# Kernel tuning notes

Measured on AMD Instinct MI355X. Metric: run time of the kernel, lower is better.

Reference implementation:

```python
import jax, jax.numpy as jnp
import numpy as np


def setup_inputs() -> dict:
    key = jax.random.key(0)
    ks = jax.random.split(key, 8)
    B, N, E, d, R = 16, 4096, 65536, 256, 4
    Vg, Vs = 30000, 20000
    x = jax.random.uniform(ks[0], (B, N, d), dtype=jnp.float32)
    W_all = jax.random.normal(ks[1], (R + 1, d, d), dtype=jnp.float32)
    Wg = jax.random.normal(ks[2], (d, Vg), dtype=jnp.float32)
    bg = jnp.zeros((Vg,), dtype=jnp.float32)
    Ws = jax.random.normal(ks[3], (d, Vs), dtype=jnp.float32)
    bs = jnp.zeros((Vs,), dtype=jnp.float32)
    edge_index = jax.random.randint(ks[4], (B, 2, E), 0, N, dtype=jnp.int64)
    edge_type = jax.random.randint(ks[5], (B, E), 0, R, dtype=jnp.int64)
    return {"x": x, "W_all": W_all, "Wg": Wg, "bg": bg, "Ws": Ws, "bs": bs,
            "edge_index": edge_index, "edge_type": edge_type}


def _rgcn_graph(xg, W_all, Wg, bg, Ws, bs, ei, et):
    # xg: [N,d], ei: [2,E], et: [E]
    N, d = xg.shape
    R = W_all.shape[0] - 1
    src, dst = ei[0], ei[1]
    # per-relation support H @ W_r (relations 1..R); W_all[0] is self-connection
    support = jnp.einsum('nd,rde->rne', xg, W_all[1:])  # [R, N, d]
    # c_ir = max(#edges of relation r with source i, 1)  (row-degree of A_r)
    deg = jnp.zeros((N, R), xg.dtype).at[src, et].add(1.0)
    c = jnp.maximum(deg, 1.0)
    # edge-wise gather-scale-scatter: out[i] += support[r, j] / c[i, r]
    w = 1.0 / c[src, et]                      # [E]
    msgs = support[et, dst] * w[:, None]      # [E, d]
    agg = jax.ops.segment_sum(msgs, src, num_segments=N)  # [N, d]
    h = jax.nn.relu(agg + xg @ W_all[0])
    x0 = h[0]                                  # current node features [d]
    logits_g = x0 @ Wg + bg
    logits_s = x0 @ Ws + bs
    return jax.nn.log_softmax(logits_g), jax.nn.log_softmax(logits_s)


def reference(x, W_all, Wg, bg, Ws, bs, edge_index, edge_type):
    f = jax.vmap(_rgcn_graph, in_axes=(0, None, None, None, None, None, 0, 0))
    return f(x, W_all, Wg, bg, Ws, bs, edge_index, edge_type)
```

## Files before the change

### kernel.cpp

```cpp
#include <hip/hip_runtime.h>
#include <math.h>

#define NB 16
#define NN 4096
#define NE 65536
#define DD 256
#define NR 4
#define VG 30000
#define VS 20000
#define NBG 118
#define NBS 79
#define MCAP 1024

#define WS_MC   0
#define WS_CNT  16
#define WS_H0A  80
#define WS_H0T  4176
#define WS_MAT  8272
#define WS_PM   24656
#define WS_PS   27808
#define WS_L    30960

__global__ __launch_bounds__(256) void k_scan(
    const int* __restrict__ ei, const int* __restrict__ etp,
    int* __restrict__ mcount, int* __restrict__ cnt, int* __restrict__ matches) {
  const int b = blockIdx.x;
  const int* src = ei + (size_t)b * 2 * NE;
  const int* dst = src + NE;
  const int* etb = etp + (size_t)b * NE;
  const int per = NE / gridDim.y;
  const int base = blockIdx.y * per;
  for (int e0 = base + threadIdx.x * 4; e0 < base + per; e0 += blockDim.x * 4) {
    const int4 s = *reinterpret_cast<const int4*>(&src[e0]);
#pragma unroll
    for (int u = 0; u < 4; ++u) {
      const int sv = (u == 0) ? s.x : (u == 1) ? s.y : (u == 2) ? s.z : s.w;
      if (sv == 0) {
        const int e = e0 + u;
        const int r = etb[e];
        const int j = dst[e];
        atomicAdd(&cnt[b * NR + r], 1);
        const int idx = atomicAdd(&mcount[b], 1);
        if (idx < MCAP) matches[b * MCAP + idx] = (r << 12) | j;
      }
    }
  }
}

__global__ __launch_bounds__(256) void k_h0(
    const float* __restrict__ x, const float* __restrict__ W_all,
    const int* __restrict__ mcount, const int* __restrict__ cnt,
    const int* __restrict__ matches, float* __restrict__ h0acc) {
  const int b = blockIdx.x;
  const int r = blockIdx.y;
  const int j = threadIdx.x;
  __shared__ float u[DD];
  if (r == 0) {
    u[j] = x[((size_t)b * NN) * DD + j];
  } else {
    float s = 0.f;
    const int n = min(mcount[b], MCAP);
    for (int m = 0; m < n; ++m) {
      const int mv = matches[b * MCAP + m];
      if ((mv >> 12) == r - 1) s += x[((size_t)b * NN + (mv & 4095)) * DD + j];
    }
    const float cinv = 1.0f / fmaxf((float)cnt[b * NR + (r - 1)], 1.0f);
    u[j] = s * cinv;
  }
  __syncthreads();
  const float* W = W_all + (size_t)r * DD * DD;
  float acc = 0.f;
#pragma unroll 2
  for (int k0 = 0; k0 < DD; k0 += 8) {
    float w[8];
#pragma unroll
    for (int q = 0; q < 8; ++q) w[q] = W[(k0 + q) * DD + j];
#pragma unroll
    for (int q = 0; q < 8; ++q) acc = fmaf(u[k0 + q], w[q], acc);
  }
  atomicAdd(&h0acc[b * DD + j], acc);
}

__global__ __launch_bounds__(256) void k_h0fin(
    const float* __restrict__ h0acc, float* __restrict__ h0T) {
  const int b = blockIdx.x;
  const int j = threadIdx.x;
  h0T[j * NB + b] = fmaxf(h0acc[b * DD + j], 0.f);
}

__global__ __launch_bounds__(256) void k_logits(
    const float* __restrict__ Wg, const float* __restrict__ bg,
    const float* __restrict__ Ws, const float* __restrict__ bs,
    const float* __restrict__ h0T, float* __restrict__ out,
    float* __restrict__ pm, float* __restrict__ ps) {
  const int blk = blockIdx.x;
  int tile, V, nblk;
  const float *W, *bias;
  float *o, *pmh, *psh;
  if (blk < NBG) {
    tile = blk; V = VG; W = Wg; bias = bg; o = out;
    pmh = pm; psh = ps; nblk = NBG;
  } else {
    tile = blk - NBG; V = VS; W = Ws; bias = bs; o = out + (size_t)NB * VG;
    pmh = pm + NB * NBG; psh = ps + NB * NBG; nblk = NBS;
  }
  const int v = tile * 256 + threadIdx.x;
  const bool valid = (v < V);
  const int vc = valid ? v : (V - 1);
  float acc[NB];
  const float bb = bias[vc];
#pragma unroll
  for (int b = 0; b < NB; ++b) acc[b] = bb;
  const float* Wv = W + vc;
#pragma unroll 2
  for (int k0 = 0; k0 < DD; k0 += 16) {
    float w[16];
#pragma unroll
    for (int u = 0; u < 16; ++u) w[u] = Wv[(size_t)(k0 + u) * V];
#pragma unroll
    for (int u = 0; u < 16; ++u) {
#pragma unroll
      for (int b = 0; b < NB; ++b)
        acc[b] = fmaf(h0T[(k0 + u) * NB + b], w[u], acc[b]);
    }
  }
  if (valid) {
#pragma unroll
    for (int b = 0; b < NB; ++b) o[(size_t)b * V + v] = acc[b];
  }
  __shared__ float redm[4][NB];
  __shared__ float reds[4][NB];
  const int lane = threadIdx.x & 63;
  const int wave = threadIdx.x >> 6;
#pragma unroll
  for (int b = 0; b < NB; ++b) {
    float m = valid ? acc[b] : -INFINITY;
    for (int off = 32; off > 0; off >>= 1) m = fmaxf(m, __shfl_xor(m, off));
    float sx = valid ? __expf(acc[b] - m) : 0.f;
    for (int off = 32; off > 0; off >>= 1) sx += __shfl_xor(sx, off);
    if (lane == 0) { redm[wave][b] = m; reds[wave][b] = sx; }
  }
  __syncthreads();
  if (threadIdx.x < NB) {
    const int b = threadIdx.x;
    float M = -INFINITY;
#pragma unroll
    for (int wv = 0; wv < 4; ++wv) M = fmaxf(M, redm[wv][b]);
    float S = 0.f;
#pragma unroll
    for (int wv = 0; wv < 4; ++wv) {
      float mi = redm[wv][b];
      S += (mi > -INFINITY) ? reds[wv][b] * __expf(mi - M) : 0.f;
    }
    pmh[b * nblk + tile] = M;
    psh[b * nblk + tile] = S;
  }
}

__global__ __launch_bounds__(1024) void k_reduce(
    const float* __restrict__ pm, const float* __restrict__ ps,
    float* __restrict__ L) {
  const int gtid = blockIdx.x * 1024 + threadIdx.x;
  const int w = gtid >> 6;
  const int lane = gtid & 63;
  const int head = w >> 4;
  const int b = w & 15;
  const float* pmh = pm + (head ? NB * NBG : 0);
  const float* psh = ps + (head ? NB * NBG : 0);
  const int nblk = head ? NBS : NBG;
  float m = -INFINITY, s = 0.f;
  for (int i = lane; i < nblk; i += 64) {
    float mi = pmh[b * nblk + i];
    float si = psh[b * nblk + i];
    float Mn = fmaxf(m, mi);
    float sn = ((m > -INFINITY) ? s * __expf(m - Mn) : 0.f) +
               ((mi > -INFINITY) ? si * __expf(mi - Mn) : 0.f);
    m = Mn; s = sn;
  }
  for (int off = 32; off > 0; off >>= 1) {
    float mo = __shfl_xor(m, off);
    float so = __shfl_xor(s, off);
    float Mn = fmaxf(m, mo);
    float sn = ((m > -INFINITY) ? s * __expf(m - Mn) : 0.f) +
               ((mo > -INFINITY) ? so * __expf(mo - Mn) : 0.f);
    m = Mn; s = sn;
  }
  if (lane == 0) L[head * NB + b] = m + logf(s);
}

__global__ __launch_bounds__(256) void k_final(
    float* __restrict__ out, const float* __restrict__ L) {
  const size_t i = (size_t)blockIdx.x * 256 + threadIdx.x;
  const size_t total = (size_t)NB * (VG + VS);
  if (i >= total) return;
  int head, b;
  if (i < (size_t)NB * VG) { head = 0; b = (int)(i / VG); }
  else { head = 1; b = (int)((i - (size_t)NB * VG) / VS); }
  out[i] -= L[head * NB + b];
}

extern "C" void kernel_launch(void* const* d_in, const int* in_sizes, int n_in,
                              void* d_out, int out_size, void* d_ws, size_t ws_size,
                              hipStream_t stream) {
  const float* x     = (const float*)d_in[0];
  const float* W_all = (const float*)d_in[1];
  const float* Wg    = (const float*)d_in[2];
  const float* bg    = (const float*)d_in[3];
  const float* Ws    = (const float*)d_in[4];
  const float* bs    = (const float*)d_in[5];
  const int*   ei    = (const int*)d_in[6];
  const int*   etp   = (const int*)d_in[7];
  float* out = (float*)d_out;
  float* ws  = (float*)d_ws;

  int*   mcount  = (int*)(ws + WS_MC);
  int*   cnt     = (int*)(ws + WS_CNT);
  float* h0acc   = ws + WS_H0A;
  float* h0T     = ws + WS_H0T;
  int*   matches = (int*)(ws + WS_MAT);
  float* pm      = ws + WS_PM;
  float* ps      = ws + WS_PS;
  float* L       = ws + WS_L;

  hipMemsetAsync(d_ws, 0, (16 + 64 + NB * DD) * sizeof(float), stream);

  dim3 gscan(NB, 16);
  k_scan<<<gscan, 256, 0, stream>>>(ei, etp, mcount, cnt, matches);
  dim3 gh0(NB, NR + 1);
  k_h0<<<gh0, 256, 0, stream>>>(x, W_all, mcount, cnt, matches, h0acc);
  k_h0fin<<<NB, 256, 0, stream>>>(h0acc, h0T);
  k_logits<<<NBG + NBS, 256, 0, stream>>>(Wg, bg, Ws, bs, h0T, out, pm, ps);
  k_reduce<<<2, 1024, 0, stream>>>(pm, ps, L);
  k_final<<<(NB * (VG + VS) + 255) / 256, 256, 0, stream>>>(out, L);
}
```

Before: 197.1 us.

## Split K across waves in logits and batch W reuse in h0 matmul

The logits kernel now gives each 64-column tile four waves that each cover a quarter of the reduction dimension. The partial sums are combined through shared memory, which raises the block count from about 197 to 782 so the GPU is better filled. The h0 computation is split into a kernel that gathers neighbor features and a matmul kernel that loads each W_r slice once for all 16 batches. Before, every batch reread the full 256x256 weight matrix. The cost is an extra launch, a round trip through workspace memory, and shared-memory reduction overhead.

```diff
diff --git a/kernel.cpp b/kernel.cpp
--- a/kernel.cpp
+++ b/kernel.cpp
@@ -8,18 +8,19 @@
 #define NR 4
 #define VG 30000
 #define VS 20000
-#define NBG 118
-#define NBS 79
+#define NBG2 469
+#define NBS2 313
 #define MCAP 1024
 
 #define WS_MC   0
 #define WS_CNT  16
 #define WS_H0A  80
-#define WS_H0T  4176
-#define WS_MAT  8272
-#define WS_PM   24656
-#define WS_PS   27808
-#define WS_L    30960
+#define WS_U    4176
+#define WS_H0T  24656
+#define WS_MAT  28752
+#define WS_PM   45136
+#define WS_PS   57648
+#define WS_L    70160
 
 __global__ __launch_bounds__(256) void k_scan(
     const int* __restrict__ ei, const int* __restrict__ etp,
@@ -47,38 +48,74 @@
   }
 }
 
-__global__ __launch_bounds__(256) void k_h0(
-    const float* __restrict__ x, const float* __restrict__ W_all,
-    const int* __restrict__ mcount, const int* __restrict__ cnt,
-    const int* __restrict__ matches, float* __restrict__ h0acc) {
+__global__ __launch_bounds__(256) void k_u(
+    const float* __restrict__ x, const int* __restrict__ mcount,
+    const int* __restrict__ cnt, const int* __restrict__ matches,
+    float* __restrict__ u) {
   const int b = blockIdx.x;
   const int r = blockIdx.y;
-  const int j = threadIdx.x;
-  __shared__ float u[DD];
+  const int k = threadIdx.x;
+  float val;
   if (r == 0) {
-    u[j] = x[((size_t)b * NN) * DD + j];
+    val = x[((size_t)b * NN) * DD + k];
   } else {
     float s = 0.f;
     const int n = min(mcount[b], MCAP);
     for (int m = 0; m < n; ++m) {
       const int mv = matches[b * MCAP + m];
-      if ((mv >> 12) == r - 1) s += x[((size_t)b * NN + (mv & 4095)) * DD + j];
-    }
-    const float cinv = 1.0f / fmaxf((float)cnt[b * NR + (r - 1)], 1.0f);
-    u[j] = s * cinv;
+      if ((mv >> 12) == r - 1) s += x[((size_t)b * NN + (mv & 4095)) * DD + k];
+    }
+    s *= 1.0f / fmaxf((float)cnt[b * NR + (r - 1)], 1.0f);
+    val = s;
+  }
+  u[((size_t)b * (NR + 1) + r) * DD + k] = val;
+}
+
+__global__ __launch_bounds__(256) void k_h0mm(
+    const float* __restrict__ W_all, const float* __restrict__ u,
+    float* __restrict__ h0acc) {
+  const int r = blockIdx.x;
+  const int jt = blockIdx.y;
+  __shared__ float us[NB * DD];
+  __shared__ float red[8][NB][32];
+#pragma unroll
+  for (int t = 0; t < 16; ++t) {
+    const int flat = t * 256 + threadIdx.x;
+    const int b = flat >> 8, k = flat & 255;
+    us[flat] = u[((size_t)b * (NR + 1) + r) * DD + k];
   }
   __syncthreads();
-  const float* W = W_all + (size_t)r * DD * DD;
-  float acc = 0.f;
-#pragma unroll 2
-  for (int k0 = 0; k0 < DD; k0 += 8) {
+  const int jl = threadIdx.x & 31;
+  const int kg = threadIdx.x >> 5;
+  const int j = jt * 32 + jl;
+  const float* W = W_all + (size_t)r * DD * DD + j;
+  float acc[NB];
+#pragma unroll
+  for (int b = 0; b < NB; ++b) acc[b] = 0.f;
+  const int kb = kg * 32;
+  for (int k0 = 0; k0 < 32; k0 += 8) {
     float w[8];
 #pragma unroll
-    for (int q = 0; q < 8; ++q) w[q] = W[(k0 + q) * DD + j];
-#pragma unroll
-    for (int q = 0; q < 8; ++q) acc = fmaf(u[k0 + q], w[q], acc);
-  }
-  atomicAdd(&h0acc[b * DD + j], acc);
+    for (int q = 0; q < 8; ++q) w[q] = W[(size_t)(kb + k0 + q) * DD];
+#pragma unroll
+    for (int q = 0; q < 8; ++q) {
+#pragma unroll
+      for (int b = 0; b < NB; ++b)
+        acc[b] = fmaf(us[b * DD + kb + k0 + q], w[q], acc[b]);
+    }
+  }
+#pragma unroll
+  for (int b = 0; b < NB; ++b) red[kg][b][jl] = acc[b];
+  __syncthreads();
+  const int bh = threadIdx.x >> 5;
+#pragma unroll
+  for (int half = 0; half < 2; ++half) {
+    const int b = bh + half * 8;
+    float s = 0.f;
+#pragma unroll
+    for (int g = 0; g < 8; ++g) s += red[g][b][jl];
+    atomicAdd(&h0acc[b * DD + jt * 32 + jl], s);
+  }
 }
 
 __global__ __launch_bounds__(256) void k_h0fin(
@@ -97,63 +134,58 @@
   int tile, V, nblk;
   const float *W, *bias;
   float *o, *pmh, *psh;
-  if (blk < NBG) {
+  if (blk < NBG2) {
     tile = blk; V = VG; W = Wg; bias = bg; o = out;
-    pmh = pm; psh = ps; nblk = NBG;
+    pmh = pm; psh = ps; nblk = NBG2;
   } else {
-    tile = blk - NBG; V = VS; W = Ws; bias = bs; o = out + (size_t)NB * VG;
-    pmh = pm + NB * NBG; psh = ps + NB * NBG; nblk = NBS;
-  }
-  const int v = tile * 256 + threadIdx.x;
+    tile = blk - NBG2; V = VS; W = Ws; bias = bs; o = out + (size_t)NB * VG;
+    pmh = pm + NB * NBG2; psh = ps + NB * NBG2; nblk = NBS2;
+  }
+  const int vl = threadIdx.x & 63;
+  const int kq = threadIdx.x >> 6;
+  const int v = tile * 64 + vl;
   const bool valid = (v < V);
   const int vc = valid ? v : (V - 1);
   float acc[NB];
-  const float bb = bias[vc];
-#pragma unroll
-  for (int b = 0; b < NB; ++b) acc[b] = bb;
+#pragma unroll
+  for (int b = 0; b < NB; ++b) acc[b] = 0.f;
   const float* Wv = W + vc;
-#pragma unroll 2
-  for (int k0 = 0; k0 < DD; k0 += 16) {
+  const int kbase = kq * 64;
+#pragma unroll
+  for (int k0 = 0; k0 < 64; k0 += 16) {
     float w[16];
 #pragma unroll
-    for (int u = 0; u < 16; ++u) w[u] = Wv[(size_t)(k0 + u) * V];
+    for (int u = 0; u < 16; ++u) w[u] = Wv[(size_t)(kbase + k0 + u) * V];
 #pragma unroll
     for (int u = 0; u < 16; ++u) {
 #pragma unroll
       for (int b = 0; b < NB; ++b)
-        acc[b] = fmaf(h0T[(k0 + u) * NB + b], w[u], acc[b]);
-    }
-  }
-  if (valid) {
-#pragma unroll
-    for (int b = 0; b < NB; ++b) o[(size_t)b * V + v] = acc[b];
-  }
-  __shared__ float redm[4][NB];
-  __shared__ float reds[4][NB];
-  const int lane = threadIdx.x & 63;
-  const int wave = threadIdx.x >> 6;
-#pragma unroll
-  for (int b = 0; b < NB; ++b) {
-    float m = valid ? acc[b] : -INFINITY;
-    for (int off = 32; off > 0; off >>= 1) m = fmaxf(m, __shfl_xor(m, off));
-    float sx = valid ? __expf(acc[b] - m) : 0.f;
-    for (int off = 32; off > 0; off >>= 1) sx += __shfl_xor(sx, off);
-    if (lane == 0) { redm[wave][b] = m; reds[wave][b] = sx; }
+        acc[b] = fmaf(h0T[(kbase + k0 + u) * NB + b], w[u], acc[b]);
+    }
+  }
+  __shared__ float red[3][NB][64];
+  if (kq > 0) {
+#pragma unroll
+    for (int b = 0; b < NB; ++b) red[kq - 1][b][vl] = acc[b];
   }
   __syncthreads();
-  if (threadIdx.x < NB) {
-    const int b = threadIdx.x;
-    float M = -INFINITY;
-#pragma unroll
-    for (int wv = 0; wv < 4; ++wv) M = fmaxf(M, redm[wv][b]);
-    float S = 0.f;
-#pragma unroll
-    for (int wv = 0; wv < 4; ++wv) {
-      float mi = redm[wv][b];
-      S += (mi > -INFINITY) ? reds[wv][b] * __expf(mi - M) : 0.f;
-    }
-    pmh[b * nblk + tile] = M;
-    psh[b * nblk + tile] = S;
+  if (kq == 0) {
+    const float bb = bias[vc];
+#pragma unroll
+    for (int b = 0; b < NB; ++b)
+      acc[b] += bb + red[0][b][vl] + red[1][b][vl] + red[2][b][vl];
+    if (valid) {
+#pragma unroll
+      for (int b = 0; b < NB; ++b) o[(size_t)b * V + v] = acc[b];
+    }
+#pragma unroll
+    for (int b = 0; b < NB; ++b) {
+      float m = valid ? acc[b] : -INFINITY;
+      for (int off = 32; off > 0; off >>= 1) m = fmaxf(m, __shfl_xor(m, off));
+      float sx = valid ? __expf(acc[b] - m) : 0.f;
+      for (int off = 32; off > 0; off >>= 1) sx += __shfl_xor(sx, off);
+      if (vl == 0) { pmh[b * nblk + tile] = m; psh[b * nblk + tile] = sx; }
+    }
   }
 }
 
@@ -165,9 +197,9 @@
   const int lane = gtid & 63;
   const int head = w >> 4;
   const int b = w & 15;
-  const float* pmh = pm + (head ? NB * NBG : 0);
-  const float* psh = ps + (head ? NB * NBG : 0);
-  const int nblk = head ? NBS : NBG;
+  const float* pmh = pm + (head ? NB * NBG2 : 0);
+  const float* psh = ps + (head ? NB * NBG2 : 0);
+  const int nblk = head ? NBS2 : NBG2;
   float m = -INFINITY, s = 0.f;
   for (int i = lane; i < nblk; i += 64) {
     float mi = pmh[b * nblk + i];
@@ -216,6 +248,7 @@
   int*   mcount  = (int*)(ws + WS_MC);
   int*   cnt     = (int*)(ws + WS_CNT);
   float* h0acc   = ws + WS_H0A;
+  float* u       = ws + WS_U;
   float* h0T     = ws + WS_H0T;
   int*   matches = (int*)(ws + WS_MAT);
   float* pm      = ws + WS_PM;
@@ -226,10 +259,12 @@
 
   dim3 gscan(NB, 16);
   k_scan<<<gscan, 256, 0, stream>>>(ei, etp, mcount, cnt, matches);
-  dim3 gh0(NB, NR + 1);
-  k_h0<<<gh0, 256, 0, stream>>>(x, W_all, mcount, cnt, matches, h0acc);
+  dim3 gu(NB, NR + 1);
+  k_u<<<gu, 256, 0, stream>>>(x, mcount, cnt, matches, u);
+  dim3 gmm(NR + 1, 8);
+  k_h0mm<<<gmm, 256, 0, stream>>>(W_all, u, h0acc);
   k_h0fin<<<NB, 256, 0, stream>>>(h0acc, h0T);
-  k_logits<<<NBG + NBS, 256, 0, stream>>>(Wg, bg, Ws, bs, h0T, out, pm, ps);
+  k_logits<<<NBG2 + NBS2, 256, 0, stream>>>(Wg, bg, Ws, bs, h0T, out, pm, ps);
   k_reduce<<<2, 1024, 0, stream>>>(pm, ps, L);
   k_final<<<(NB * (VG + VS) + 255) / 256, 256, 0, stream>>>(out, L);
 }
```

Result: no change. 197.0 us (-0.0%).
